# Performance work log

Hardware: AMD Instinct MI355X
Metric: run time of the kernel (lower is better)

## Reference

```python
import jax, jax.numpy as jnp
import numpy as np

TEMPERATURE = 0.1
NORMALIZED = True


def _l2norm(x, eps=1e-12):
    # matches F.normalize(p=2, dim=1)
    n = jnp.sqrt(jnp.sum(x * x, axis=1, keepdims=True))
    return x / jnp.maximum(n, eps)


def setup_inputs() -> dict:
    key = jax.random.key(0)
    k1, k2, k3, k4 = jax.random.split(key, 4)
    B, D = 4096, 256
    return {
        "hs": jax.random.normal(k1, (B, D), dtype=jnp.float32),
        "ht0": jax.random.normal(k2, (B, D), dtype=jnp.float32),
        "ht1": jax.random.normal(k3, (B, D), dtype=jnp.float32),
        "labels": jax.random.randint(k4, (B,), 0, 100, dtype=jnp.int64)
        if jax.config.jax_enable_x64 else jax.random.randint(k4, (B,), 0, 100, dtype=jnp.int32),
        "num_views": 2,
    }


def _per_teacher_loss(hs_n, ht_n, mask, logits_mask, batch_size, num_views):
    # features: [N, D] with N = 2B
    features = jnp.concatenate([hs_n, ht_n], axis=0)
    sim = jnp.matmul(features, features.T) / TEMPERATURE          # [N, N]
    exp_logits = jnp.exp(sim) * logits_mask                        # [N, N]
    log_prob = sim - jnp.log(jnp.sum(exp_logits, axis=1, keepdims=True))
    per_inst = -jnp.sum(mask * log_prob, axis=1) / jnp.sum(mask, axis=1)  # [N]
    if num_views > 1:
        per_inst = per_inst.reshape(batch_size, num_views).mean(axis=1)
    return per_inst.mean()


def reference(hs, ht0, ht1, labels, num_views):
    batch_size = labels.shape[0]
    hs = hs.reshape(batch_size, -1)
    ht_list = [ht0.reshape(batch_size, -1), ht1.reshape(batch_size, -1)]
    if NORMALIZED:
        hs = _l2norm(hs)
        ht_list = [_l2norm(ht) for ht in ht_list]

    labels2 = jnp.concatenate([labels, labels])                    # [N]
    mask = (labels2[:, None] == labels2[None, :]).astype(jnp.float32)
    N = 2 * batch_size
    logits_mask = 1.0 - jnp.eye(N, dtype=jnp.float32)              # zero diagonal
    mask = mask * logits_mask

    inter_loss = 0.0
    for ht in ht_list:
        inter_loss = inter_loss + _per_teacher_loss(
            hs, ht, mask, logits_mask, batch_size, num_views)
    return inter_loss / len(ht_list)
```

## Files before the change

kernel.cpp:

```cpp
#include <hip/hip_runtime.h>
#include <hip/hip_bf16.h>

#define B_SIZE 4096
#define D_SIZE 256
#define N_SIZE 8192
#define LOG2E10 14.4269504089f

#if __has_builtin(__builtin_amdgcn_exp2f)
#define FAST_EXP2(x) __builtin_amdgcn_exp2f(x)
#else
#define FAST_EXP2(x) exp2f(x)
#endif

typedef __attribute__((ext_vector_type(8))) short short8;
typedef __attribute__((ext_vector_type(4))) short short4v;
typedef __attribute__((ext_vector_type(4))) float floatx4;


__device__ __forceinline__ void async16(void* lds, const void* g) {
    __builtin_amdgcn_global_load_lds(
        (const __attribute__((address_space(1))) unsigned int*)g,
        (__attribute__((address_space(3))) unsigned int*)lds, 16, 0, 0);
}

__device__ __forceinline__ void pair_from_q(int q, int& R, int& C) {
    int r = (int)((1.0f + sqrtf(1.0f + 8.0f * (float)q)) * 0.5f);
    while (r * (r + 1) / 2 > q) --r;
    while ((r + 1) * (r + 2) / 2 <= q) ++r;
    R = r; C = q - r * (r + 1) / 2;
}

__global__ void norm_kernel(const float* __restrict__ hs,
                            const float* __restrict__ ht0,
                            const float* __restrict__ ht1,
                            __hip_bfloat16* __restrict__ dst,
                            float* __restrict__ zero_region) {
    const int tid = threadIdx.x;
    const int wv  = tid >> 6;
    const int l   = tid & 63;
    const int gid = blockIdx.x * 256 + tid;
    if (gid < 16386) zero_region[gid] = 0.0f;

    const int row = blockIdx.x * 4 + wv;
    const float* src = (row < 4096) ? (hs + row * D_SIZE)
                     : (row < 8192) ? (ht0 + (row - 4096) * D_SIZE)
                                    : (ht1 + (row - 8192) * D_SIZE);
    floatx4 x = *reinterpret_cast<const floatx4*>(src + l * 4);
    float ss = x[0] * x[0] + x[1] * x[1] + x[2] * x[2] + x[3] * x[3];
#pragma unroll
    for (int off = 32; off > 0; off >>= 1) ss += __shfl_xor(ss, off);
    float inv = 1.0f / fmaxf(sqrtf(ss), 1e-12f);
    short4v o;
#pragma unroll
    for (int k = 0; k < 4; ++k) {
        __hip_bfloat16 h = __float2bfloat16(x[k] * inv);
        o[k] = *reinterpret_cast<short*>(&h);
    }
    *reinterpret_cast<short4v*>(dst + row * D_SIZE + l * 4) = o;
}

__global__ __launch_bounds__(256, 2)
void sim_kernel(const __hip_bfloat16* __restrict__ featS,
                const __hip_bfloat16* __restrict__ featT0,
                const __hip_bfloat16* __restrict__ featT1,
                float* __restrict__ Sarr) {
    __shared__ __align__(16) unsigned char sB[2][32768];

    const int p = blockIdx.x;
    const int t = blockIdx.y;
    const __hip_bfloat16* featT = t ? featT1 : featT0;

    int R, C;
    pair_from_q(p, R, C);

    const int tid  = threadIdx.x;
    const int w    = tid >> 6;
    const int l    = tid & 63;
    const int quad = l >> 4;
    const int lcol = l & 15;
    const int row_base = R * 256 + w * 64;

    short8 af[4][8];
#pragma unroll
    for (int rt = 0; rt < 4; ++rt) {
        int arow = row_base + rt * 16 + lcol;
        const __hip_bfloat16* ap = (arow < B_SIZE) ? featS + arow * D_SIZE
                                                   : featT + (arow - B_SIZE) * D_SIZE;
#pragma unroll
        for (int ks = 0; ks < 8; ++ks)
            af[rt][ks] = *reinterpret_cast<const short8*>(ap + ks * 32 + quad * 8);
    }

    float Sp[4][4];
#pragma unroll
    for (int rt = 0; rt < 4; ++rt)
#pragma unroll
        for (int r = 0; r < 4; ++r) Sp[rt][r] = 0.0f;

    const int col0 = C * 256;

    auto stage = [&](int b, int cb) {
        int tb = cb + w * 16;
        const __hip_bfloat16* cp = (tb < B_SIZE) ? featS + tb * D_SIZE
                                                 : featT + (tb - B_SIZE) * D_SIZE;
        const char* gp = (const char*)cp + (l & 15) * 512 + (l >> 4) * 16;
        unsigned char* lp = &sB[b][w * 8192];
#pragma unroll
        for (int ks = 0; ks < 8; ++ks)
            async16(lp + ks * 1024, gp + ks * 64);
    };

    stage(0, col0);

    for (int g = 0; g < 4; ++g) {
        const int buf = g & 1;
        __syncthreads();
        if (g + 1 < 4) stage(buf ^ 1, col0 + (g + 1) * 64);

        const int gcol = col0 + g * 64;
        if (gcol > row_base) continue;
        const bool dg = (gcol == row_base);

        float Cp[4] = {0.f, 0.f, 0.f, 0.f};
#pragma unroll
        for (int up = 0; up < 2; ++up) {
            floatx4 acc[2][4];
#pragma unroll
            for (int j = 0; j < 2; ++j)
#pragma unroll
                for (int rt = 0; rt < 4; ++rt) acc[j][rt] = floatx4{0.f, 0.f, 0.f, 0.f};

#pragma unroll
            for (int ks = 0; ks < 8; ++ks) {
                short8 bf[2];
#pragma unroll
                for (int j = 0; j < 2; ++j)
                    bf[j] = *reinterpret_cast<const short8*>(
                        &sB[buf][(up * 2 + j) * 8192 + ks * 1024 + l * 16]);
#pragma unroll
                for (int j = 0; j < 2; ++j)
#pragma unroll
                    for (int rt = 0; rt < 4; ++rt)
                        acc[j][rt] = __builtin_amdgcn_mfma_f32_16x16x32_bf16(
                            af[rt][ks], bf[j], acc[j][rt], 0, 0, 0);
            }
#pragma unroll
            for (int j = 0; j < 2; ++j)
#pragma unroll
                for (int rt = 0; rt < 4; ++rt)
#pragma unroll
                    for (int r = 0; r < 4; ++r) {
                        float e = FAST_EXP2(acc[j][rt][r] * LOG2E10);
                        Sp[rt][r] += e;
                        Cp[up * 2 + j] += e;
                    }
        }

        if (!dg) {
#pragma unroll
            for (int u = 0; u < 4; ++u) {
                Cp[u] += __shfl_xor(Cp[u], 16);
                Cp[u] += __shfl_xor(Cp[u], 32);
            }
            if (quad == 0) {
#pragma unroll
                for (int u = 0; u < 4; ++u)
                    atomicAdd(&Sarr[t * N_SIZE + gcol + u * 16 + lcol], Cp[u]);
            }
        }
    }

#pragma unroll
    for (int rt = 0; rt < 4; ++rt)
#pragma unroll
        for (int r = 0; r < 4; ++r) {
#pragma unroll
            for (int m = 1; m < 16; m <<= 1) Sp[rt][r] += __shfl_xor(Sp[rt][r], m);
        }
    if (lcol == 0) {
#pragma unroll
        for (int rt = 0; rt < 4; ++rt)
#pragma unroll
            for (int r = 0; r < 4; ++r) {
                int row = row_base + rt * 16 + quad * 4 + r;
                atomicAdd(&Sarr[t * N_SIZE + row], Sp[rt][r]);
            }
    }
}

__global__ void classstat_kernel(const __hip_bfloat16* __restrict__ featS,
                                 const __hip_bfloat16* __restrict__ featT0,
                                 const __hip_bfloat16* __restrict__ featT1,
                                 const int* __restrict__ labels,
                                 const float* __restrict__ Sarr,
                                 float* __restrict__ lossAcc,
                                 int* __restrict__ ticket,
                                 float* __restrict__ out) {
    __shared__ int idx[256];
    __shared__ int nsh;
    __shared__ float gS[256], gT0[256], gT1[256];
    __shared__ float wpart[4];

    const int c   = blockIdx.x;
    const int tid = threadIdx.x;
    const int wv  = tid >> 6;
    const int l   = tid & 63;

    if (tid == 0) nsh = 0;
    __syncthreads();
    for (int i = tid; i < B_SIZE; i += 256)
        if ((labels[i] & 127) == c) { int p = atomicAdd(&nsh, 1); idx[p] = i; }
    __syncthreads();
    const int n = nsh;

    if (n > 0) {
        float aS = 0.f, a0 = 0.f, a1 = 0.f;
        for (int m = 0; m < n; ++m) {
            int r = idx[m] * D_SIZE + tid;
            aS += __bfloat162float(featS[r]);
            a0 += __bfloat162float(featT0[r]);
            a1 += __bfloat162float(featT1[r]);
        }
        gS[tid] = aS; gT0[tid] = a0; gT1[tid] = a1;
    }
    __syncthreads();

    float psum = 0.0f;
    const float M = 2.0f * (float)n - 1.0f;
    for (int inst = wv; inst < 4 * n; inst += 4) {
        const int t    = inst & 1;
        const int half = (inst >> 1) & 1;
        const int i    = idx[inst >> 2];
        const __hip_bfloat16* f = half ? ((t ? featT1 : featT0) + i * D_SIZE)
                                       : (featS + i * D_SIZE);
        short4v fb = *reinterpret_cast<const short4v*>(f + l * 4);
        const float* gT = t ? gT1 : gT0;
        float dot = 0.f, aii = 0.f;
#pragma unroll
        for (int k = 0; k < 4; ++k) {
            unsigned int u = ((unsigned int)(unsigned short)fb[k]) << 16;
            float fx = __uint_as_float(u);
            dot += fx * (gS[l * 4 + k] + gT[l * 4 + k]);
            aii += fx * fx;
        }
#pragma unroll
        for (int m = 1; m < 64; m <<= 1) {
            dot += __shfl_xor(dot, m);
            aii += __shfl_xor(aii, m);
        }
        if (l == 0) {
            int row = half ? (B_SIZE + i) : i;
            float S = Sarr[t * N_SIZE + row];
            float E = FAST_EXP2(LOG2E10 * aii);
            psum += logf(S - E) - 10.0f * (dot - aii) / M;
        }
    }
    if (l == 0) wpart[wv] = psum;
    __syncthreads();
    if (tid == 0) {
        atomicAdd(lossAcc, wpart[0] + wpart[1] + wpart[2] + wpart[3]);
        __threadfence();
        if (atomicAdd(ticket, 1) == 127) {
            float tot = atomicAdd(lossAcc, 0.0f);
            out[0] = tot / 16384.0f;
        }
    }
}

extern "C" void kernel_launch(void* const* d_in, const int* in_sizes, int n_in,
                              void* d_out, int out_size, void* d_ws, size_t ws_size,
                              hipStream_t stream) {
    const float* hs     = (const float*)d_in[0];
    const float* ht0    = (const float*)d_in[1];
    const float* ht1    = (const float*)d_in[2];
    const int*   labels = (const int*)d_in[3];

    char* ws = (char*)d_ws;
    float* Sarr    = (float*)(ws);
    float* lossAcc = (float*)(ws + 65536);
    int*   ticket  = (int*)(ws + 65540);
    __hip_bfloat16* featS  = (__hip_bfloat16*)(ws + 524288);
    __hip_bfloat16* featT0 = (__hip_bfloat16*)(ws + 524288 + 2097152);
    __hip_bfloat16* featT1 = (__hip_bfloat16*)(ws + 524288 + 2 * 2097152);

    norm_kernel<<<3072, 256, 0, stream>>>(hs, ht0, ht1, featS, (float*)ws);
    sim_kernel<<<dim3(528, 2), 256, 0, stream>>>(featS, featT0, featT1, Sarr);
    classstat_kernel<<<128, 256, 0, stream>>>(featS, featT0, featT1, labels,
                                              Sarr, lossAcc, ticket, (float*)d_out);
}
```

Before: 167.2 us.

## Restructure sim kernel to 512-thread blocks with smaller per-wave tiles

The similarity kernel now uses 8 waves per block, each owning 32 rows instead of 64. It stages 32-column B chunks into a halved LDS buffer over 8 iterations, which cuts per-wave register use (fewer A fragments and accumulators). The grid is flattened: off-diagonal tile pairs are listed first and diagonal tiles last, and the triangular index mapping changes accordingly. The class-statistics kernel spreads the per-class feature sums across waves with vectorized loads and LDS atomics instead of one serial loop per thread. The trade-off is more barriers and smaller MFMA work per sync, in exchange for higher occupancy and better load balance.

After: 175.0 us. 4.7% more time.

```diff
diff --git a/kernel.cpp b/kernel.cpp
--- a/kernel.cpp
+++ b/kernel.cpp
@@ -25,9 +25,9 @@
 
 __device__ __forceinline__ void pair_from_q(int q, int& R, int& C) {
     int r = (int)((1.0f + sqrtf(1.0f + 8.0f * (float)q)) * 0.5f);
-    while (r * (r + 1) / 2 > q) --r;
-    while ((r + 1) * (r + 2) / 2 <= q) ++r;
-    R = r; C = q - r * (r + 1) / 2;
+    while (r * (r - 1) / 2 > q) --r;
+    while ((r + 1) * r / 2 <= q) ++r;
+    R = r; C = q - r * (r - 1) / 2;
 }
 
 __global__ void norm_kernel(const float* __restrict__ hs,
@@ -59,30 +59,35 @@
     *reinterpret_cast<short4v*>(dst + row * D_SIZE + l * 4) = o;
 }
 
-__global__ __launch_bounds__(256, 2)
+__global__ __launch_bounds__(512, 2)
 void sim_kernel(const __hip_bfloat16* __restrict__ featS,
                 const __hip_bfloat16* __restrict__ featT0,
                 const __hip_bfloat16* __restrict__ featT1,
                 float* __restrict__ Sarr) {
-    __shared__ __align__(16) unsigned char sB[2][32768];
-
-    const int p = blockIdx.x;
-    const int t = blockIdx.y;
+    __shared__ __align__(16) unsigned char sB[2][16384];
+
+    int R, C, t;
+    if (blockIdx.x < 992) {
+        t = blockIdx.x & 1;
+        pair_from_q(blockIdx.x >> 1, R, C);
+    } else {
+        int i = blockIdx.x - 992;
+        t = i & 1;
+        R = C = i >> 1;
+    }
     const __hip_bfloat16* featT = t ? featT1 : featT0;
-
-    int R, C;
-    pair_from_q(p, R, C);
 
     const int tid  = threadIdx.x;
     const int w    = tid >> 6;
     const int l    = tid & 63;
     const int quad = l >> 4;
     const int lcol = l & 15;
-    const int row_base = R * 256 + w * 64;
-
-    short8 af[4][8];
-#pragma unroll
-    for (int rt = 0; rt < 4; ++rt) {
+    const int row_base = R * 256 + w * 32;
+    const int col0 = C * 256;
+
+    short8 af[2][8];
+#pragma unroll
+    for (int rt = 0; rt < 2; ++rt) {
         int arow = row_base + rt * 16 + lcol;
         const __hip_bfloat16* ap = (arow < B_SIZE) ? featS + arow * D_SIZE
                                                    : featT + (arow - B_SIZE) * D_SIZE;
@@ -91,87 +96,87 @@
             af[rt][ks] = *reinterpret_cast<const short8*>(ap + ks * 32 + quad * 8);
     }
 
-    float Sp[4][4];
-#pragma unroll
-    for (int rt = 0; rt < 4; ++rt)
+    float Sp[2][4];
+#pragma unroll
+    for (int rt = 0; rt < 2; ++rt)
 #pragma unroll
         for (int r = 0; r < 4; ++r) Sp[rt][r] = 0.0f;
 
-    const int col0 = C * 256;
-
     auto stage = [&](int b, int cb) {
-        int tb = cb + w * 16;
+        const int u   = w & 1;
+        const int ks0 = (w >> 1) * 2;
+        const int tb  = cb + u * 16;
         const __hip_bfloat16* cp = (tb < B_SIZE) ? featS + tb * D_SIZE
                                                  : featT + (tb - B_SIZE) * D_SIZE;
         const char* gp = (const char*)cp + (l & 15) * 512 + (l >> 4) * 16;
-        unsigned char* lp = &sB[b][w * 8192];
-#pragma unroll
-        for (int ks = 0; ks < 8; ++ks)
+        unsigned char* lp = &sB[b][u * 8192];
+#pragma unroll
+        for (int kk = 0; kk < 2; ++kk) {
+            int ks = ks0 + kk;
             async16(lp + ks * 1024, gp + ks * 64);
+        }
     };
 
     stage(0, col0);
 
-    for (int g = 0; g < 4; ++g) {
+    for (int g = 0; g < 8; ++g) {
         const int buf = g & 1;
         __syncthreads();
-        if (g + 1 < 4) stage(buf ^ 1, col0 + (g + 1) * 64);
-
-        const int gcol = col0 + g * 64;
+        if (g + 1 < 8) stage(buf ^ 1, col0 + (g + 1) * 32);
+
+        const int gcol = col0 + g * 32;
         if (gcol > row_base) continue;
         const bool dg = (gcol == row_base);
 
-        float Cp[4] = {0.f, 0.f, 0.f, 0.f};
-#pragma unroll
-        for (int up = 0; up < 2; ++up) {
-            floatx4 acc[2][4];
+        floatx4 acc[2][2];
+#pragma unroll
+        for (int j = 0; j < 2; ++j)
+#pragma unroll
+            for (int rt = 0; rt < 2; ++rt) acc[j][rt] = floatx4{0.f, 0.f, 0.f, 0.f};
+
+#pragma unroll
+        for (int ks = 0; ks < 8; ++ks) {
+            short8 bf[2];
 #pragma unroll
             for (int j = 0; j < 2; ++j)
-#pragma unroll
-                for (int rt = 0; rt < 4; ++rt) acc[j][rt] = floatx4{0.f, 0.f, 0.f, 0.f};
-
-#pragma unroll
-            for (int ks = 0; ks < 8; ++ks) {
-                short8 bf[2];
-#pragma unroll
-                for (int j = 0; j < 2; ++j)
-                    bf[j] = *reinterpret_cast<const short8*>(
-                        &sB[buf][(up * 2 + j) * 8192 + ks * 1024 + l * 16]);
-#pragma unroll
-                for (int j = 0; j < 2; ++j)
-#pragma unroll
-                    for (int rt = 0; rt < 4; ++rt)
-                        acc[j][rt] = __builtin_amdgcn_mfma_f32_16x16x32_bf16(
-                            af[rt][ks], bf[j], acc[j][rt], 0, 0, 0);
-            }
+                bf[j] = *reinterpret_cast<const short8*>(
+                    &sB[buf][j * 8192 + ks * 1024 + l * 16]);
 #pragma unroll
             for (int j = 0; j < 2; ++j)
 #pragma unroll
-                for (int rt = 0; rt < 4; ++rt)
-#pragma unroll
-                    for (int r = 0; r < 4; ++r) {
-                        float e = FAST_EXP2(acc[j][rt][r] * LOG2E10);
-                        Sp[rt][r] += e;
-                        Cp[up * 2 + j] += e;
-                    }
-        }
+                for (int rt = 0; rt < 2; ++rt)
+                    acc[j][rt] = __builtin_amdgcn_mfma_f32_16x16x32_bf16(
+                        af[rt][ks], bf[j], acc[j][rt], 0, 0, 0);
+        }
+
+        float Cp[2] = {0.f, 0.f};
+#pragma unroll
+        for (int j = 0; j < 2; ++j)
+#pragma unroll
+            for (int rt = 0; rt < 2; ++rt)
+#pragma unroll
+                for (int r = 0; r < 4; ++r) {
+                    float e = FAST_EXP2(acc[j][rt][r] * LOG2E10);
+                    Sp[rt][r] += e;
+                    Cp[j] += e;
+                }
 
         if (!dg) {
 #pragma unroll
-            for (int u = 0; u < 4; ++u) {
-                Cp[u] += __shfl_xor(Cp[u], 16);
-                Cp[u] += __shfl_xor(Cp[u], 32);
+            for (int j = 0; j < 2; ++j) {
+                Cp[j] += __shfl_xor(Cp[j], 16);
+                Cp[j] += __shfl_xor(Cp[j], 32);
             }
             if (quad == 0) {
 #pragma unroll
-                for (int u = 0; u < 4; ++u)
-                    atomicAdd(&Sarr[t * N_SIZE + gcol + u * 16 + lcol], Cp[u]);
+                for (int j = 0; j < 2; ++j)
+                    atomicAdd(&Sarr[t * N_SIZE + gcol + j * 16 + lcol], Cp[j]);
             }
         }
     }
 
 #pragma unroll
-    for (int rt = 0; rt < 4; ++rt)
+    for (int rt = 0; rt < 2; ++rt)
 #pragma unroll
         for (int r = 0; r < 4; ++r) {
 #pragma unroll
@@ -179,7 +184,7 @@
         }
     if (lcol == 0) {
 #pragma unroll
-        for (int rt = 0; rt < 4; ++rt)
+        for (int rt = 0; rt < 2; ++rt)
 #pragma unroll
             for (int r = 0; r < 4; ++r) {
                 int row = row_base + rt * 16 + quad * 4 + r;
@@ -207,21 +212,33 @@
     const int l   = tid & 63;
 
     if (tid == 0) nsh = 0;
+    gS[tid] = 0.f; gT0[tid] = 0.f; gT1[tid] = 0.f;
     __syncthreads();
     for (int i = tid; i < B_SIZE; i += 256)
         if ((labels[i] & 127) == c) { int p = atomicAdd(&nsh, 1); idx[p] = i; }
     __syncthreads();
     const int n = nsh;
 
-    if (n > 0) {
-        float aS = 0.f, a0 = 0.f, a1 = 0.f;
-        for (int m = 0; m < n; ++m) {
-            int r = idx[m] * D_SIZE + tid;
-            aS += __bfloat162float(featS[r]);
-            a0 += __bfloat162float(featT0[r]);
-            a1 += __bfloat162float(featT1[r]);
-        }
-        gS[tid] = aS; gT0[tid] = a0; gT1[tid] = a1;
+    {
+        float aS[4] = {0,0,0,0}, a0[4] = {0,0,0,0}, a1[4] = {0,0,0,0};
+        for (int m = wv; m < n; m += 4) {
+            int base = idx[m] * D_SIZE + l * 4;
+            short4v bS = *reinterpret_cast<const short4v*>(featS + base);
+            short4v b0 = *reinterpret_cast<const short4v*>(featT0 + base);
+            short4v b1 = *reinterpret_cast<const short4v*>(featT1 + base);
+#pragma unroll
+            for (int k = 0; k < 4; ++k) {
+                aS[k] += __uint_as_float(((unsigned int)(unsigned short)bS[k]) << 16);
+                a0[k] += __uint_as_float(((unsigned int)(unsigned short)b0[k]) << 16);
+                a1[k] += __uint_as_float(((unsigned int)(unsigned short)b1[k]) << 16);
+            }
+        }
+#pragma unroll
+        for (int k = 0; k < 4; ++k) {
+            atomicAdd(&gS[l * 4 + k],  aS[k]);
+            atomicAdd(&gT0[l * 4 + k], a0[k]);
+            atomicAdd(&gT1[l * 4 + k], a1[k]);
+        }
     }
     __syncthreads();
 
@@ -238,8 +255,7 @@
         float dot = 0.f, aii = 0.f;
 #pragma unroll
         for (int k = 0; k < 4; ++k) {
-            unsigned int u = ((unsigned int)(unsigned short)fb[k]) << 16;
-            float fx = __uint_as_float(u);
+            float fx = __uint_as_float(((unsigned int)(unsigned short)fb[k]) << 16);
             dot += fx * (gS[l * 4 + k] + gT[l * 4 + k]);
             aii += fx * fx;
         }
@@ -284,7 +300,7 @@
     __hip_bfloat16* featT1 = (__hip_bfloat16*)(ws + 524288 + 2 * 2097152);
 
     norm_kernel<<<3072, 256, 0, stream>>>(hs, ht0, ht1, featS, (float*)ws);
-    sim_kernel<<<dim3(528, 2), 256, 0, stream>>>(featS, featT0, featT1, Sarr);
+    sim_kernel<<<1056, 512, 0, stream>>>(featS, featT0, featT1, Sarr);
     classstat_kernel<<<128, 256, 0, stream>>>(featS, featT0, featT1, labels,
                                               Sarr, lossAcc, ticket, (float*)d_out);
 }
```
